# Kernel optimization log

Measured on AMD Instinct MI355X. Metric: run time of the kernel, lower is better.

The kernel has to match this reference:

```python
import jax, jax.numpy as jnp
import numpy as np

D = 256                      # covariance dim, hardcoded by bottleneck Conv2d(_, 256, 1)
ITER_N = 5                   # SqrtmLayer(output, 5)
_r, _c = np.triu_indices(D)
FLAT_IDX = jnp.asarray(_r * D + _c)   # upper-tri (incl. diag) indices into flattened d*d


def setup_inputs() -> dict:
    key = jax.random.key(0)
    ks = jax.random.split(key, 5)
    B, C, H, W = 64, 2048, 16, 16
    num_classes = 4
    feats = D * (D + 1) // 2  # 32896
    return {
        "features": jax.random.normal(ks[0], (B, C, H, W), jnp.float32),
        "w_bn": jax.random.normal(ks[1], (D, C), jnp.float32) * 0.02,
        "b_bn": jnp.zeros((D,), jnp.float32),
        "w_type": jax.random.normal(ks[2], (num_classes, feats), jnp.float32) * 0.01,
        "b_type": jnp.zeros((num_classes,), jnp.float32),
        "w_flag": jax.random.normal(ks[3], (1, feats), jnp.float32) * 0.01,
        "b_flag": jnp.zeros((1,), jnp.float32),
    }


def _covpool(x):
    # x: [B, d, h, w] -> second-order pooling: x_f @ I_hat @ x_f^T, equivalent
    # to (1/M) * centered @ centered^T  (I_hat = -1/M^2 * ones + 1/M * eye)
    B, d, h, w = x.shape
    M = h * w
    xf = x.reshape(B, d, M)
    centered = xf - xf.mean(axis=2, keepdims=True)
    return jnp.einsum('bim,bjm->bij', centered, centered) / M  # [B, d, d]


def _sqrtm_ns(A, iter_n=ITER_N):
    # Newton-Schulz iteration for matrix square root (iSQRT-COV style)
    B, d, _ = A.shape
    I3 = 3.0 * jnp.eye(d, dtype=A.dtype)
    normA = jnp.trace(A, axis1=1, axis2=2)          # [B], pre-normalization
    An = A / normA[:, None, None]
    ZY = 0.5 * (I3 - An)
    Y = jnp.matmul(An, ZY)
    Z = ZY
    for _ in range(iter_n - 2):
        ZY = 0.5 * (I3 - jnp.matmul(Z, Y))
        Y = jnp.matmul(Y, ZY)
        Z = jnp.matmul(ZY, Z)
    YZY = 0.5 * jnp.matmul(Y, I3 - jnp.matmul(Z, Y))
    return YZY * jnp.sqrt(normA)[:, None, None]     # post-compensation


def reference(features, w_bn, b_bn, w_type, b_type, w_flag, b_flag):
    # 1x1 bottleneck conv: [B, C, H, W] -> [B, 256, H, W]
    x = jnp.einsum('bchw,oc->bohw', features, w_bn) + b_bn[None, :, None, None]
    cov = _covpool(x)                # [B, 256, 256]
    s = _sqrtm_ns(cov)               # [B, 256, 256]
    B = s.shape[0]
    vec = s.reshape(B, D * D)[:, FLAT_IDX]   # triu-vec: [B, 32896]
    type_logits = vec @ w_type.T + b_type    # [B, num_classes]
    flag_logits = vec @ w_flag.T + b_flag    # [B, 1]
    return (type_logits, flag_logits)
```

## Files before the change

### kernel.cpp

```cpp
#include <hip/hip_runtime.h>
#include <math.h>


typedef __attribute__((ext_vector_type(8))) short bf16x8;
typedef __attribute__((ext_vector_type(4))) float f32x4;
typedef __attribute__((ext_vector_type(4))) unsigned u32x4;
typedef __attribute__((ext_vector_type(2))) unsigned u32x2;

__device__ __forceinline__ unsigned fbits(float f) { union { float f; unsigned u; } x; x.f = f; return x.u; }
__device__ __forceinline__ float bitsf(unsigned u) { union { float f; unsigned u; } x; x.u = u; return x.f; }
__device__ __forceinline__ float bf16v(short h) { return bitsf(((unsigned)(unsigned short)h) << 16); }

__device__ __forceinline__ unsigned pack_h(float a, float b) {
  return (fbits(a) >> 16) | (fbits(b) & 0xFFFF0000u);
}
__device__ __forceinline__ unsigned pack_l(float a, float b) {
  float la = a - bitsf(fbits(a) & 0xFFFF0000u);
  float lb = b - bitsf(fbits(b) & 0xFFFF0000u);
  return (fbits(la) >> 16) | (fbits(lb) & 0xFFFF0000u);
}

__device__ __forceinline__ const bf16x8* fragp(const char* M, int kt, int row,
                                               int g, int pl) {
  return (const bf16x8*)(M + (size_t)kt * 32768 + (size_t)row * 128 +
                         ((((pl << 2) + g) ^ (row & 7)) << 4));
}
__device__ __forceinline__ const bf16x8* fragl(const char* L, int kt, int row,
                                               int g, int pl) {
  return (const bf16x8*)(L + kt * 8192 + row * 128 +
                         ((((pl << 2) + g) ^ (row & 7)) << 4));
}

__device__ __forceinline__ void write_quad_g(char* M, int row, int k0,
                                             const float* v) {
  char* rp = M + (size_t)(k0 >> 5) * 32768 + (size_t)row * 128;
  const int s = (k0 & 31) >> 3, bo = (k0 & 7) * 2;
  *(u32x2*)(rp + (((s) ^ (row & 7)) << 4) + bo) =
      (u32x2){pack_h(v[0], v[1]), pack_h(v[2], v[3])};
  *(u32x2*)(rp + (((s + 4) ^ (row & 7)) << 4) + bo) =
      (u32x2){pack_l(v[0], v[1]), pack_l(v[2], v[3])};
}
__device__ __forceinline__ void write_quad_l(char* L, int row, int k0,
                                             const float* v) {
  char* rp = L + (k0 >> 5) * 8192 + row * 128;
  const int s = (k0 & 31) >> 3, bo = (k0 & 7) * 2;
  *(u32x2*)(rp + (((s) ^ (row & 7)) << 4) + bo) =
      (u32x2){pack_h(v[0], v[1]), pack_h(v[2], v[3])};
  *(u32x2*)(rp + (((s + 4) ^ (row & 7)) << 4) + bo) =
      (u32x2){pack_l(v[0], v[1]), pack_l(v[2], v[3])};
}
__device__ __forceinline__ void read_quad_g(const char* M, int row, int k0,
                                            float* v) {
  const char* rp = M + (size_t)(k0 >> 5) * 32768 + (size_t)row * 128;
  const int s = (k0 & 31) >> 3, bo = (k0 & 7) * 2;
  const u32x2 hq = *(const u32x2*)(rp + (((s) ^ (row & 7)) << 4) + bo);
  const u32x2 lq = *(const u32x2*)(rp + (((s + 4) ^ (row & 7)) << 4) + bo);
  v[0] = bitsf(hq[0] << 16) + bitsf(lq[0] << 16);
  v[1] = bitsf(hq[0] & 0xFFFF0000u) + bitsf(lq[0] & 0xFFFF0000u);
  v[2] = bitsf(hq[1] << 16) + bitsf(lq[1] << 16);
  v[3] = bitsf(hq[1] & 0xFFFF0000u) + bitsf(lq[1] & 0xFFFF0000u);
}

#define MFMA3(c, aH, aL, bH, bL)                                            \
  c = __builtin_amdgcn_mfma_f32_16x16x32_bf16(aL, bH, c, 0, 0, 0);          \
  c = __builtin_amdgcn_mfma_f32_16x16x32_bf16(aH, bL, c, 0, 0, 0);          \
  c = __builtin_amdgcn_mfma_f32_16x16x32_bf16(aH, bH, c, 0, 0, 0);

#define LGKM_BAR() do { asm volatile("s_waitcnt lgkmcnt(0)" ::: "memory"); \
                        __builtin_amdgcn_s_barrier(); } while (0)

__global__ __launch_bounds__(256) void prep_k(
    const float* __restrict__ w_bn, const float* __restrict__ w_type,
    const float* __restrict__ w_flag, char* __restrict__ Wf,
    float* __restrict__ W2)
{
  const int bid = blockIdx.x;
  if (bid < 64) {
    const int kt = bid, r = threadIdx.x;
    const float* src = w_bn + (size_t)r * 2048 + kt * 32;
    char* rp = Wf + (size_t)kt * 32768 + (size_t)r * 128;
#pragma unroll
    for (int s = 0; s < 4; ++s) {
      float x[8];
#pragma unroll
      for (int e = 0; e < 8; ++e) x[e] = src[s * 8 + e];
      *(u32x4*)(rp + ((s ^ (r & 7)) << 4)) =
          (u32x4){pack_h(x[0], x[1]), pack_h(x[2], x[3]),
                  pack_h(x[4], x[5]), pack_h(x[6], x[7])};
      *(u32x4*)(rp + (((s + 4) ^ (r & 7)) << 4)) =
          (u32x4){pack_l(x[0], x[1]), pack_l(x[2], x[3]),
                  pack_l(x[4], x[5]), pack_l(x[6], x[7])};
    }
  } else {
    const int idx = bid - 64;
    const int v = idx >> 6, chunk = idx & 63;
    const float* src = (v < 4) ? (w_type + (size_t)v * 32896) : w_flag;
    const int e0 = chunk * 1024 + threadIdx.x * 4;
#pragma unroll
    for (int q = 0; q < 4; ++q) {
      const int e = e0 + q;
      const int i = e >> 8, j = e & 255;
      const int r = i < j ? i : j, c = i < j ? j : i;
      const int t = r * 256 - (r * (r - 1)) / 2 + (c - r);
      W2[(size_t)v * 65536 + e] = src[t] * (i == j ? 1.0f : 0.5f);
    }
  }
}

__global__ __launch_bounds__(512) void conv6_k(
    const char* __restrict__ Wf, const float* __restrict__ F,
    float* __restrict__ Xpart)
{
  __shared__ float bf32s[2][64 * 33];
  __shared__ __align__(16) char bfmt[2][2][8192];

  const int tid = threadIdx.x, lane = tid & 63, w = tid >> 6;
  const int wr = w >> 1, wc = w & 1, fr = lane & 15, g = lane >> 4;
  const int jb = blockIdx.x * 64, bz = blockIdx.y, ks = blockIdx.z;
  const int kb = ks * 32;
  const float* Fb = F + (size_t)bz * 524288;

  const int blc = tid >> 4, blpx = (tid & 15) * 4;
  const int pkpx = tid >> 3, pkq = tid & 3, pkpl = (tid >> 2) & 1;

  f32x4 acc[4][2] = {};
  bf16x8 paA[4][2], paB[4][2];

  auto bload = [&](int t) -> float4 {
    return *(const float4*)(Fb + ((size_t)(kb + t) * 32 + blc) * 256 + jb + blpx);
  };
  auto bf32w = [&](int kk, const float4& r) {
    float* p = &bf32s[kk][0];
    p[(blpx + 0) * 33 + blc] = r.x;
    p[(blpx + 1) * 33 + blc] = r.y;
    p[(blpx + 2) * 33 + blc] = r.z;
    p[(blpx + 3) * 33 + blc] = r.w;
  };
  auto aload = [&](int t, bf16x8 (*pa)[2]) {
#pragma unroll
    for (int m = 0; m < 4; ++m) {
      const int r = wr * 64 + m * 16 + fr;
#pragma unroll
      for (int pl = 0; pl < 2; ++pl) pa[m][pl] = *fragp(Wf, kb + t, r, g, pl);
    }
  };
  auto pack = [&](int kk, int dq) {
    const float* p = &bf32s[kk][pkpx * 33 + pkq * 8];
    float x[8];
#pragma unroll
    for (int e = 0; e < 8; ++e) x[e] = p[e];
    u32x4 outv;
    if (pkpl == 0)
      outv = (u32x4){pack_h(x[0], x[1]), pack_h(x[2], x[3]),
                     pack_h(x[4], x[5]), pack_h(x[6], x[7])};
    else
      outv = (u32x4){pack_l(x[0], x[1]), pack_l(x[2], x[3]),
                     pack_l(x[4], x[5]), pack_l(x[6], x[7])};
    const int slot = ((pkpl << 2) + pkq) ^ (pkpx & 7);
    *(u32x4*)(&bfmt[dq][kk][pkpx * 128 + slot * 16]) = outv;
  };
  auto gemmstep = [&](int sq, int kk, bf16x8 (*pa)[2]) {
    bf16x8 bH[2], bL[2];
#pragma unroll
    for (int n = 0; n < 2; ++n) {
      const int r = wc * 32 + n * 16 + fr;
      const char* rp = &bfmt[sq][kk][r * 128];
      bH[n] = *(const bf16x8*)(rp + ((g ^ (r & 7)) << 4));
      bL[n] = *(const bf16x8*)(rp + (((g + 4) ^ (r & 7)) << 4));
    }
#pragma unroll
    for (int m = 0; m < 4; ++m)
#pragma unroll
      for (int n = 0; n < 2; ++n) {
        f32x4 c = acc[m][n];
        MFMA3(c, pa[m][0], pa[m][1], bH[n], bL[n]);
        acc[m][n] = c;
      }
  };

  float4 b0 = bload(0), b1 = bload(1), b2 = bload(2), b3 = bload(3);
  float4 blE0 = bload(4), blE1 = bload(5);
  float4 blO0 = bload(6), blO1 = bload(7);
  aload(0, paA);
  aload(1, paB);

  bf32w(0, b0); bf32w(1, b1);
  LGKM_BAR();
  pack(0, 0); pack(1, 0);
  LGKM_BAR();
  bf32w(0, b2); bf32w(1, b3);
  LGKM_BAR();

  for (int pp = 0; pp < 8; ++pp) {
    const int k4 = 4 * pp;
    gemmstep(0, 0, paA);
    gemmstep(0, 1, paB);
    aload(k4 + 2, paA);
    aload(k4 + 3, paB);
    pack(0, 1); pack(1, 1);
    LGKM_BAR();
    if (pp < 7) { bf32w(0, blE0); bf32w(1, blE1); }
    if (pp < 6) { blE0 = bload(k4 + 8); blE1 = bload(k4 + 9); }
    LGKM_BAR();
    gemmstep(1, 0, paA);
    gemmstep(1, 1, paB);
    if (pp < 7) { aload(k4 + 4, paA); aload(k4 + 5, paB); }
    if (pp < 7) { pack(0, 0); pack(1, 0); }
    LGKM_BAR();
    if (pp < 7) { bf32w(0, blO0); bf32w(1, blO1); }
    if (pp < 6) { blO0 = bload(k4 + 10); blO1 = bload(k4 + 11); }
    LGKM_BAR();
  }

  float* Xp = Xpart + ((size_t)ks * 64 + bz) * 65536;
#pragma unroll
  for (int m = 0; m < 4; ++m) {
    const int gi0 = wr * 64 + m * 16 + g * 4;
#pragma unroll
    for (int n = 0; n < 2; ++n) {
      const int gj = jb + wc * 32 + n * 16 + fr;
#pragma unroll
      for (int j = 0; j < 4; ++j)
        Xp[(size_t)(gi0 + j) * 256 + gj] = acc[m][n][j];
    }
  }
}

__global__ __launch_bounds__(256) void combine_k(
    const float* __restrict__ Xp0, const float* __restrict__ Xp1,
    const float* __restrict__ bias, char* __restrict__ X,
    float* __restrict__ mu, float* __restrict__ nrm_part)
{
  const int chunk = blockIdx.x, bz = blockIdx.y;
  const int tid = threadIdx.x, lane = tid & 63, w = tid >> 6;
  const float* p0 = Xp0 + (size_t)bz * 65536;
  const float* p1 = Xp1 + (size_t)bz * 65536;
  char* Xb = X + (size_t)bz * 262144;
  float tracc = 0.f;
#pragma unroll
  for (int i = 0; i < 8; ++i) {
    const int r = chunk * 32 + w * 8 + i;
    const float4 a = *(const float4*)(p0 + (size_t)r * 256 + lane * 4);
    const float4 b = *(const float4*)(p1 + (size_t)r * 256 + lane * 4);
    const float bi = bias[r];
    float v[4] = {a.x + b.x + bi, a.y + b.y + bi,
                  a.z + b.z + bi, a.w + b.w + bi};
    float s = v[0] + v[1] + v[2] + v[3];
    float ss = v[0] * v[0] + v[1] * v[1] + v[2] * v[2] + v[3] * v[3];
#pragma unroll
    for (int o = 32; o > 0; o >>= 1) {
      s += __shfl_down(s, o);
      ss += __shfl_down(ss, o);
    }
    const float st = __shfl(s, 0), sst = __shfl(ss, 0);
    const float m = st * (1.f / 256.f);
    if (lane == 0) mu[bz * 256 + r] = m;
    tracc += sst * (1.f / 256.f) - m * m;
    write_quad_g(Xb, r, lane * 4, v);
  }
  __shared__ float red[4];
  if (lane == 0) red[w] = tracc;
  __syncthreads();
  if (tid == 0)
    nrm_part[bz * 8 + chunk] = red[0] + red[1] + red[2] + red[3];
}

__device__ __forceinline__ float nrm_sum(const float* nrmp, int bz) {
  float nv = 0.f;
#pragma unroll
  for (int q = 0; q < 8; ++q) nv += nrmp[bz * 8 + q];
  return nv;
}

template <int MODE>
__global__ __launch_bounds__(512) void col_k(
    const char* __restrict__ A1, const char* __restrict__ Bsrc,
    const char* __restrict__ Ys, const char* __restrict__ Zs,
    char* __restrict__ outA, char* __restrict__ outB,
    const float* __restrict__ mu, const float* __restrict__ nrmp,
    float* __restrict__ Sf)
{
  __shared__ __align__(16) char Plds[65536];
  const int tid = threadIdx.x, lane = tid & 63, w = tid >> 6;
  const int fr = lane & 15, g = lane >> 4;
  const int blk = blockIdx.x;
  const int bz = (blk & 7) * 8 + ((blk >> 3) & 7);
  const int jb = (blk >> 6) * 64;
  const size_t MB = 262144;
  const char* Ab = A1 + (size_t)bz * MB;
  const char* Bb = Bsrc + (size_t)bz * MB;
  const int r0 = g * 4;

  f32x4 acc[2][4] = {};
  {
    bf16x8 pa[2][2][2], pb[2][4][2];
#pragma unroll
    for (int par = 0; par < 2; ++par) {
#pragma unroll
      for (int m = 0; m < 2; ++m) {
        const int r = w * 32 + m * 16 + fr;
#pragma unroll
        for (int pl = 0; pl < 2; ++pl) pa[par][m][pl] = *fragp(Ab, par, r, g, pl);
      }
#pragma unroll
      for (int n = 0; n < 4; ++n) {
        const int r = jb + n * 16 + fr;
#pragma unroll
        for (int pl = 0; pl < 2; ++pl) pb[par][n][pl] = *fragp(Bb, par, r, g, pl);
      }
    }
    for (int t2 = 0; t2 < 8; t2 += 2) {
#pragma unroll
      for (int par = 0; par < 2; ++par) {
        const int t = t2 + par;
        bf16x8 aH[2], aL[2], bH[4], bL[4];
#pragma unroll
        for (int m = 0; m < 2; ++m) { aH[m] = pa[par][m][0]; aL[m] = pa[par][m][1]; }
#pragma unroll
        for (int n = 0; n < 4; ++n) { bH[n] = pb[par][n][0]; bL[n] = pb[par][n][1]; }
        if (t + 2 < 8) {
#pragma unroll
          for (int m = 0; m < 2; ++m) {
            const int r = w * 32 + m * 16 + fr;
#pragma unroll
            for (int pl = 0; pl < 2; ++pl)
              pa[par][m][pl] = *fragp(Ab, t + 2, r, g, pl);
          }
#pragma unroll
          for (int n = 0; n < 4; ++n) {
            const int r = jb + n * 16 + fr;
#pragma unroll
            for (int pl = 0; pl < 2; ++pl)
              pb[par][n][pl] = *fragp(Bb, t + 2, r, g, pl);
          }
        }
#pragma unroll
        for (int m = 0; m < 2; ++m)
#pragma unroll
          for (int n = 0; n < 4; ++n) {
            f32x4 c = acc[m][n];
            MFMA3(c, aH[m], aL[m], bH[n], bL[n]);
            acc[m][n] = c;
          }
      }
    }
  }

  if constexpr (MODE == 0) {
    const float rn = 1.0f / nrm_sum(nrmp, bz);
    const float* mub = mu + bz * 256;
    char* oA = outA + (size_t)bz * MB;
    char* oB = outB + (size_t)bz * MB;
#pragma unroll
    for (int m = 0; m < 2; ++m) {
      const int gi0 = w * 32 + m * 16 + r0;
#pragma unroll
      for (int n = 0; n < 4; ++n) {
        const int gj = jb + n * 16 + fr;
        float vv[4], zz[4];
#pragma unroll
        for (int j = 0; j < 4; ++j) {
          const float v =
              (acc[m][n][j] * (1.f / 256.f) - mub[gi0 + j] * mub[gj]) * rn;
          vv[j] = v;
          zz[j] = (gi0 + j == gj ? 1.5f : 0.f) - 0.5f * v;
        }
        write_quad_g(oA, gj, gi0, vv);
        write_quad_g(oB, gj, gi0, zz);
      }
    }
  } else if constexpr (MODE == 1) {
    char* oA = outA + (size_t)bz * MB;
#pragma unroll
    for (int m = 0; m < 2; ++m) {
      const int gi0 = w * 32 + m * 16 + r0;
#pragma unroll
      for (int n = 0; n < 4; ++n) {
        const int gj = jb + n * 16 + fr;
        float av[4], vv[4];
        read_quad_g(Bb, gj, gi0, av);
#pragma unroll
        for (int j = 0; j < 4; ++j) vv[j] = 1.5f * av[j] - 0.5f * acc[m][n][j];
        write_quad_g(oA, gj, gi0, vv);
      }
    }
  } else {
#pragma unroll
    for (int m = 0; m < 2; ++m) {
      const int gi0 = w * 32 + m * 16 + r0;
#pragma unroll
      for (int n = 0; n < 4; ++n) {
        const int jl = n * 16 + fr;
        float vv[4] = {acc[m][n][0], acc[m][n][1], acc[m][n][2], acc[m][n][3]};
        write_quad_l(Plds, jl, gi0, vv);
      }
    }
    const char* Yb = Ys + (size_t)bz * MB;
    const char* Zb = (MODE == 2) ? (Zs + (size_t)bz * MB) : nullptr;
    bf16x8 py[2][2][2], pz[2][2][2];
#pragma unroll
    for (int par = 0; par < 2; ++par)
#pragma unroll
      for (int m = 0; m < 2; ++m) {
        const int r = w * 32 + m * 16 + fr;
#pragma unroll
        for (int pl = 0; pl < 2; ++pl) {
          py[par][m][pl] = *fragp(Yb, par, r, g, pl);
          if constexpr (MODE == 2) pz[par][m][pl] = *fragp(Zb, par, r, g, pl);
        }
      }
    __syncthreads();

    f32x4 aY[2][4] = {}, aZ[2][4] = {};
    for (int t2 = 0; t2 < 8; t2 += 2) {
#pragma unroll
      for (int par = 0; par < 2; ++par) {
        const int t = t2 + par;
        bf16x8 yH[2], yL[2], zH[2], zL[2];
#pragma unroll
        for (int m = 0; m < 2; ++m) {
          yH[m] = py[par][m][0]; yL[m] = py[par][m][1];
          if constexpr (MODE == 2) { zH[m] = pz[par][m][0]; zL[m] = pz[par][m][1]; }
        }
        if (t + 2 < 8) {
#pragma unroll
          for (int m = 0; m < 2; ++m) {
            const int r = w * 32 + m * 16 + fr;
#pragma unroll
            for (int pl = 0; pl < 2; ++pl) {
              py[par][m][pl] = *fragp(Yb, t + 2, r, g, pl);
              if constexpr (MODE == 2) pz[par][m][pl] = *fragp(Zb, t + 2, r, g, pl);
            }
          }
        }
        bf16x8 bH[4], bL[4];
#pragma unroll
        for (int n = 0; n < 4; ++n) {
          const int jl = n * 16 + fr;
          bH[n] = *fragl(Plds, t, jl, g, 0);
          bL[n] = *fragl(Plds, t, jl, g, 1);
        }
#pragma unroll
        for (int m = 0; m < 2; ++m)
#pragma unroll
          for (int n = 0; n < 4; ++n) {
            f32x4 cy = aY[m][n];
            MFMA3(cy, yH[m], yL[m], bH[n], bL[n]);
            aY[m][n] = cy;
            if constexpr (MODE == 2) {
              f32x4 cz = aZ[m][n];
              MFMA3(cz, zH[m], zL[m], bH[n], bL[n]);
              aZ[m][n] = cz;
            }
          }
      }
    }
    if constexpr (MODE == 2) {
      char* oA = outA + (size_t)bz * MB;
      char* oB = outB + (size_t)bz * MB;
#pragma unroll
      for (int m = 0; m < 2; ++m) {
        const int gi0 = w * 32 + m * 16 + r0;
#pragma unroll
        for (int n = 0; n < 4; ++n) {
          const int gj = jb + n * 16 + fr;
          float base[4], vv[4];
          read_quad_g(Yb, gj, gi0, base);
#pragma unroll
          for (int j = 0; j < 4; ++j) vv[j] = 1.5f * base[j] - 0.5f * aY[m][n][j];
          write_quad_g(oA, gj, gi0, vv);
          read_quad_g(Zb, gj, gi0, base);
#pragma unroll
          for (int j = 0; j < 4; ++j) vv[j] = 1.5f * base[j] - 0.5f * aZ[m][n][j];
          write_quad_g(oB, gj, gi0, vv);
        }
      }
    } else {
      const float sq = sqrtf(nrm_sum(nrmp, bz));
      float* Sb = Sf + (size_t)bz * 65536;
#pragma unroll
      for (int m = 0; m < 2; ++m) {
        const int gi0 = w * 32 + m * 16 + r0;
#pragma unroll
        for (int n = 0; n < 4; ++n) {
          const int gj = jb + n * 16 + fr;
          float base[4];
          read_quad_g(Yb, gj, gi0, base);
          f32x4 vv;
#pragma unroll
          for (int j = 0; j < 4; ++j)
            vv[j] = (1.5f * base[j] - 0.5f * aY[m][n][j]) * sq;
          *(f32x4*)(Sb + (size_t)gj * 256 + gi0) = vv;
        }
      }
    }
  }
}

__global__ __launch_bounds__(256) void head2(
    const float* __restrict__ Sf, const float* __restrict__ W2,
    const float* __restrict__ b_type, const float* __restrict__ b_flag,
    float* __restrict__ out)
{
  const int b = blockIdx.x, v = blockIdx.y, tid = threadIdx.x;
  const float4* s4 = (const float4*)(Sf + (size_t)b * 65536);
  const float4* w4 = (const float4*)(W2 + (size_t)v * 65536);
  float acc = 0.f;
  for (int i = tid; i < 16384; i += 256) {
    const float4 a = s4[i], c = w4[i];
    acc += a.x * c.x + a.y * c.y + a.z * c.z + a.w * c.w;
  }
  __shared__ float red[256];
  red[tid] = acc;
  __syncthreads();
  for (int o = 128; o > 0; o >>= 1) {
    if (tid < o) red[tid] += red[tid + o];
    __syncthreads();
  }
  if (tid == 0) {
    if (v < 4) out[b * 4 + v] = red[0] + b_type[v];
    else       out[256 + b] = red[0] + b_flag[0];
  }
}

extern "C" void kernel_launch(void* const* d_in, const int* in_sizes, int n_in,
                              void* d_out, int out_size, void* d_ws, size_t ws_size,
                              hipStream_t stream)
{
  const float* features = (const float*)d_in[0];
  const float* w_bn     = (const float*)d_in[1];
  const float* b_bn     = (const float*)d_in[2];
  const float* w_type   = (const float*)d_in[3];
  const float* b_type   = (const float*)d_in[4];
  const float* w_flag   = (const float*)d_in[5];
  const float* b_flag   = (const float*)d_in[6];
  float* out = (float*)d_out;

  char* W = (char*)d_ws;
  const size_t PB = 16777216;
  char* P0 = W;           char* P1 = W + PB;     char* P2 = W + 2 * PB;
  char* P3 = W + 3 * PB;  char* P4 = W + 4 * PB;
  char* Wf = W + 5 * PB;
  float* W2 = (float*)(W + 5 * PB + 2097152);
  float* mu = (float*)(W + 5 * PB + 4194304);
  float* nrm_part = mu + 16384;
  float* Xpart = (float*)(W + 5 * PB + 8388608);
  float* Sf = (float*)P4;

  prep_k<<<dim3(384), dim3(256), 0, stream>>>(w_bn, w_type, w_flag, Wf, W2);
  conv6_k<<<dim3(4, 64, 2), dim3(512), 0, stream>>>(Wf, features, Xpart);
  combine_k<<<dim3(8, 64), dim3(256), 0, stream>>>(
      Xpart, Xpart + 64ull * 65536, b_bn, P0, mu, nrm_part);

  const dim3 cg(256), cb(512);
  col_k<0><<<cg, cb, 0, stream>>>(P0, P0, nullptr, nullptr, P1, P2, mu, nrm_part, nullptr);
  col_k<1><<<cg, cb, 0, stream>>>(P1, P1, nullptr, nullptr, P3, nullptr, nullptr, nullptr, nullptr);
  col_k<2><<<cg, cb, 0, stream>>>(P2, P3, P3, P2, P0, P4, nullptr, nullptr, nullptr);
  col_k<2><<<cg, cb, 0, stream>>>(P4, P0, P0, P4, P1, P2, nullptr, nullptr, nullptr);
  col_k<2><<<cg, cb, 0, stream>>>(P2, P1, P1, P2, P3, P0, nullptr, nullptr, nullptr);
  col_k<3><<<cg, cb, 0, stream>>>(P0, P3, P3, nullptr, nullptr, nullptr, nullptr, nrm_part, Sf);

  head2<<<dim3(64, 5), dim3(256), 0, stream>>>(Sf, W2, b_type, b_flag, out);
  (void)in_sizes; (void)n_in; (void)out_size; (void)ws_size;
}
```

Baseline: 274.4 us.

## Halve col_k column tile to double grid, permute W2 to match coalesced S writes

Each col_k block now covers 32 output columns instead of 64, so the grid grows from 256 to 512 blocks and LDS use per block halves, which spreads the Newton-Schulz matmuls over more CUs. The final-stage S output is written in a per-thread contiguous layout instead of row-major. prep_k permutes the head weights W2 into that same order so head2's dot product stays correct. The cost is that A-side fragments are reloaded by twice as many blocks, and the prep indexing becomes more complex.

```diff
diff --git a/kernel.cpp b/kernel.cpp
--- a/kernel.cpp
+++ b/kernel.cpp
@@ -25,9 +25,9 @@
   return (const bf16x8*)(M + (size_t)kt * 32768 + (size_t)row * 128 +
                          ((((pl << 2) + g) ^ (row & 7)) << 4));
 }
-__device__ __forceinline__ const bf16x8* fragl(const char* L, int kt, int row,
-                                               int g, int pl) {
-  return (const bf16x8*)(L + kt * 8192 + row * 128 +
+__device__ __forceinline__ const bf16x8* fragl32(const char* L, int kt, int row,
+                                                 int g, int pl) {
+  return (const bf16x8*)(L + kt * 4096 + row * 128 +
                          ((((pl << 2) + g) ^ (row & 7)) << 4));
 }
 
@@ -40,9 +40,9 @@
   *(u32x2*)(rp + (((s + 4) ^ (row & 7)) << 4) + bo) =
       (u32x2){pack_l(v[0], v[1]), pack_l(v[2], v[3])};
 }
-__device__ __forceinline__ void write_quad_l(char* L, int row, int k0,
-                                             const float* v) {
-  char* rp = L + (k0 >> 5) * 8192 + row * 128;
+__device__ __forceinline__ void write_quad_l32(char* L, int row, int k0,
+                                               const float* v) {
+  char* rp = L + (k0 >> 5) * 4096 + row * 128;
   const int s = (k0 & 31) >> 3, bo = (k0 & 7) * 2;
   *(u32x2*)(rp + (((s) ^ (row & 7)) << 4) + bo) =
       (u32x2){pack_h(v[0], v[1]), pack_h(v[2], v[3])};
@@ -93,17 +93,27 @@
     }
   } else {
     const int idx = bid - 64;
-    const int v = idx >> 6, chunk = idx & 63;
+    const int v = idx >> 4, chunk = idx & 15;
     const float* src = (v < 4) ? (w_type + (size_t)v * 32896) : w_flag;
-    const int e0 = chunk * 1024 + threadIdx.x * 4;
-#pragma unroll
-    for (int q = 0; q < 4; ++q) {
-      const int e = e0 + q;
-      const int i = e >> 8, j = e & 255;
-      const int r = i < j ? i : j, c = i < j ? j : i;
-      const int t = r * 256 - (r * (r - 1)) / 2 + (c - r);
-      W2[(size_t)v * 65536 + e] = src[t] * (i == j ? 1.0f : 0.5f);
-    }
+    const int s0 = chunk * 4096 + threadIdx.x * 16;
+    float outv[16];
+#pragma unroll
+    for (int q = 0; q < 16; ++q) {
+      const int s = s0 + q;
+      const int jbp = s >> 13, r = s & 8191;
+      const int ttid = r >> 4, qq = r & 15;
+      const int m = qq >> 3, n = (qq >> 2) & 1, jj = qq & 3;
+      const int ww = ttid >> 6, ll = ttid & 63;
+      const int i = ww * 32 + m * 16 + (ll >> 4) * 4 + jj;
+      const int jcol = jbp * 32 + n * 16 + (ll & 15);
+      const int rr = i < jcol ? i : jcol, cc = i < jcol ? jcol : i;
+      const int t = rr * 256 - (rr * (rr - 1)) / 2 + (cc - rr);
+      outv[q] = src[t] * (i == jcol ? 1.0f : 0.5f);
+    }
+    float* dst = W2 + (size_t)v * 65536 + s0;
+#pragma unroll
+    for (int q = 0; q < 4; ++q)
+      *(f32x4*)(dst + q * 4) = *(f32x4*)(outv + q * 4);
   }
 }
 
@@ -280,20 +290,21 @@
     const float* __restrict__ mu, const float* __restrict__ nrmp,
     float* __restrict__ Sf)
 {
-  __shared__ __align__(16) char Plds[65536];
+  __shared__ __align__(16) char Plds[32768];
   const int tid = threadIdx.x, lane = tid & 63, w = tid >> 6;
   const int fr = lane & 15, g = lane >> 4;
   const int blk = blockIdx.x;
   const int bz = (blk & 7) * 8 + ((blk >> 3) & 7);
-  const int jb = (blk >> 6) * 64;
+  const int jbp = blk >> 6;
+  const int jb = jbp * 32;
   const size_t MB = 262144;
   const char* Ab = A1 + (size_t)bz * MB;
   const char* Bb = Bsrc + (size_t)bz * MB;
   const int r0 = g * 4;
 
-  f32x4 acc[2][4] = {};
+  f32x4 acc[2][2] = {};
   {
-    bf16x8 pa[2][2][2], pb[2][4][2];
+    bf16x8 pa[2][2][2], pb[2][2][2];
 #pragma unroll
     for (int par = 0; par < 2; ++par) {
 #pragma unroll
@@ -303,7 +314,7 @@
         for (int pl = 0; pl < 2; ++pl) pa[par][m][pl] = *fragp(Ab, par, r, g, pl);
       }
 #pragma unroll
-      for (int n = 0; n < 4; ++n) {
+      for (int n = 0; n < 2; ++n) {
         const int r = jb + n * 16 + fr;
 #pragma unroll
         for (int pl = 0; pl < 2; ++pl) pb[par][n][pl] = *fragp(Bb, par, r, g, pl);
@@ -313,11 +324,11 @@
 #pragma unroll
       for (int par = 0; par < 2; ++par) {
         const int t = t2 + par;
-        bf16x8 aH[2], aL[2], bH[4], bL[4];
+        bf16x8 aH[2], aL[2], bH[2], bL[2];
 #pragma unroll
         for (int m = 0; m < 2; ++m) { aH[m] = pa[par][m][0]; aL[m] = pa[par][m][1]; }
 #pragma unroll
-        for (int n = 0; n < 4; ++n) { bH[n] = pb[par][n][0]; bL[n] = pb[par][n][1]; }
+        for (int n = 0; n < 2; ++n) { bH[n] = pb[par][n][0]; bL[n] = pb[par][n][1]; }
         if (t + 2 < 8) {
 #pragma unroll
           for (int m = 0; m < 2; ++m) {
@@ -327,7 +338,7 @@
               pa[par][m][pl] = *fragp(Ab, t + 2, r, g, pl);
           }
 #pragma unroll
-          for (int n = 0; n < 4; ++n) {
+          for (int n = 0; n < 2; ++n) {
             const int r = jb + n * 16 + fr;
 #pragma unroll
             for (int pl = 0; pl < 2; ++pl)
@@ -337,7 +348,7 @@
 #pragma unroll
         for (int m = 0; m < 2; ++m)
 #pragma unroll
-          for (int n = 0; n < 4; ++n) {
+          for (int n = 0; n < 2; ++n) {
             f32x4 c = acc[m][n];
             MFMA3(c, aH[m], aL[m], bH[n], bL[n]);
             acc[m][n] = c;
@@ -355,7 +366,7 @@
     for (int m = 0; m < 2; ++m) {
       const int gi0 = w * 32 + m * 16 + r0;
 #pragma unroll
-      for (int n = 0; n < 4; ++n) {
+      for (int n = 0; n < 2; ++n) {
         const int gj = jb + n * 16 + fr;
         float vv[4], zz[4];
 #pragma unroll
@@ -375,7 +386,7 @@
     for (int m = 0; m < 2; ++m) {
       const int gi0 = w * 32 + m * 16 + r0;
 #pragma unroll
-      for (int n = 0; n < 4; ++n) {
+      for (int n = 0; n < 2; ++n) {
         const int gj = jb + n * 16 + fr;
         float av[4], vv[4];
         read_quad_g(Bb, gj, gi0, av);
@@ -389,10 +400,10 @@
     for (int m = 0; m < 2; ++m) {
       const int gi0 = w * 32 + m * 16 + r0;
 #pragma unroll
-      for (int n = 0; n < 4; ++n) {
+      for (int n = 0; n < 2; ++n) {
         const int jl = n * 16 + fr;
         float vv[4] = {acc[m][n][0], acc[m][n][1], acc[m][n][2], acc[m][n][3]};
-        write_quad_l(Plds, jl, gi0, vv);
+        write_quad_l32(Plds, jl, gi0, vv);
       }
     }
     const char* Yb = Ys + (size_t)bz * MB;
@@ -411,7 +422,7 @@
       }
     __syncthreads();
 
-    f32x4 aY[2][4] = {}, aZ[2][4] = {};
+    f32x4 aY[2][2] = {}, aZ[2][2] = {};
     for (int t2 = 0; t2 < 8; t2 += 2) {
 #pragma unroll
       for (int par = 0; par < 2; ++par) {
@@ -433,17 +444,17 @@
             }
           }
         }
-        bf16x8 bH[4], bL[4];
-#pragma unroll
-        for (int n = 0; n < 4; ++n) {
+        bf16x8 bH[2], bL[2];
+#pragma unroll
+        for (int n = 0; n < 2; ++n) {
           const int jl = n * 16 + fr;
-          bH[n] = *fragl(Plds, t, jl, g, 0);
-          bL[n] = *fragl(Plds, t, jl, g, 1);
+          bH[n] = *fragl32(Plds, t, jl, g, 0);
+          bL[n] = *fragl32(Plds, t, jl, g, 1);
         }
 #pragma unroll
         for (int m = 0; m < 2; ++m)
 #pragma unroll
-          for (int n = 0; n < 4; ++n) {
+          for (int n = 0; n < 2; ++n) {
             f32x4 cy = aY[m][n];
             MFMA3(cy, yH[m], yL[m], bH[n], bL[n]);
             aY[m][n] = cy;
@@ -462,7 +473,7 @@
       for (int m = 0; m < 2; ++m) {
         const int gi0 = w * 32 + m * 16 + r0;
 #pragma unroll
-        for (int n = 0; n < 4; ++n) {
+        for (int n = 0; n < 2; ++n) {
           const int gj = jb + n * 16 + fr;
           float base[4], vv[4];
           read_quad_g(Yb, gj, gi0, base);
@@ -477,12 +488,12 @@
       }
     } else {
       const float sq = sqrtf(nrm_sum(nrmp, bz));
-      float* Sb = Sf + (size_t)bz * 65536;
+      float* Sb = Sf + (size_t)bz * 65536 + (size_t)jbp * 8192 + (size_t)tid * 16;
 #pragma unroll
       for (int m = 0; m < 2; ++m) {
         const int gi0 = w * 32 + m * 16 + r0;
 #pragma unroll
-        for (int n = 0; n < 4; ++n) {
+        for (int n = 0; n < 2; ++n) {
           const int gj = jb + n * 16 + fr;
           float base[4];
           read_quad_g(Yb, gj, gi0, base);
@@ -490,7 +501,7 @@
 #pragma unroll
           for (int j = 0; j < 4; ++j)
             vv[j] = (1.5f * base[j] - 0.5f * aY[m][n][j]) * sq;
-          *(f32x4*)(Sb + (size_t)gj * 256 + gi0) = vv;
+          *(f32x4*)(Sb + m * 8 + n * 4) = vv;
         }
       }
     }
@@ -547,12 +558,12 @@
   float* Xpart = (float*)(W + 5 * PB + 8388608);
   float* Sf = (float*)P4;
 
-  prep_k<<<dim3(384), dim3(256), 0, stream>>>(w_bn, w_type, w_flag, Wf, W2);
+  prep_k<<<dim3(144), dim3(256), 0, stream>>>(w_bn, w_type, w_flag, Wf, W2);
   conv6_k<<<dim3(4, 64, 2), dim3(512), 0, stream>>>(Wf, features, Xpart);
   combine_k<<<dim3(8, 64), dim3(256), 0, stream>>>(
       Xpart, Xpart + 64ull * 65536, b_bn, P0, mu, nrm_part);
 
-  const dim3 cg(256), cb(512);
+  const dim3 cg(512), cb(512);
   col_k<0><<<cg, cb, 0, stream>>>(P0, P0, nullptr, nullptr, P1, P2, mu, nrm_part, nullptr);
   col_k<1><<<cg, cb, 0, stream>>>(P1, P1, nullptr, nullptr, P3, nullptr, nullptr, nullptr, nullptr);
   col_k<2><<<cg, cb, 0, stream>>>(P2, P3, P3, P2, P0, P4, nullptr, nullptr, nullptr);
```

After: 286.2 us. 1.04x slower.

## Split col_k row range across two blocks and permute head weights to match output layout

Applied to the files above, without the earlier changes.

Doubles the col_k grid from 256 to 512 blocks by splitting each 64-column tile's 256 output rows into two 128-row halves, so each wave computes 16 rows instead of 32. This raises parallelism and occupancy on the GPU's many CUs, at the cost of reloading the B operand twice and, in modes 2/3, recomputing the stage-1 product for the full tile in each half. The final Sf store is rewritten as contiguous per-thread writes in a fragment-ordered layout, and prep_k permutes W2 into the same order so head2's dot product stays correct. The stage-1 redundancy in modes 2 and 3 adds MFMA work.

```diff
diff --git a/kernel.cpp b/kernel.cpp
--- a/kernel.cpp
+++ b/kernel.cpp
@@ -9,7 +9,6 @@
 
 __device__ __forceinline__ unsigned fbits(float f) { union { float f; unsigned u; } x; x.f = f; return x.u; }
 __device__ __forceinline__ float bitsf(unsigned u) { union { float f; unsigned u; } x; x.u = u; return x.f; }
-__device__ __forceinline__ float bf16v(short h) { return bitsf(((unsigned)(unsigned short)h) << 16); }
 
 __device__ __forceinline__ unsigned pack_h(float a, float b) {
   return (fbits(a) >> 16) | (fbits(b) & 0xFFFF0000u);
@@ -93,17 +92,26 @@
     }
   } else {
     const int idx = bid - 64;
-    const int v = idx >> 6, chunk = idx & 63;
+    const int v = idx >> 4, chunk = idx & 15;
     const float* src = (v < 4) ? (w_type + (size_t)v * 32896) : w_flag;
-    const int e0 = chunk * 1024 + threadIdx.x * 4;
-#pragma unroll
-    for (int q = 0; q < 4; ++q) {
-      const int e = e0 + q;
-      const int i = e >> 8, j = e & 255;
-      const int r = i < j ? i : j, c = i < j ? j : i;
-      const int t = r * 256 - (r * (r - 1)) / 2 + (c - r);
-      W2[(size_t)v * 65536 + e] = src[t] * (i == j ? 1.0f : 0.5f);
-    }
+    const int s0 = chunk * 4096 + threadIdx.x * 16;
+    float outv[16];
+#pragma unroll
+    for (int q = 0; q < 16; ++q) {
+      const int s = s0 + q;
+      const int jbp = s >> 14, rh = (s >> 13) & 1;
+      const int ttid = (s >> 4) & 511, n = (s >> 2) & 3, jj = s & 3;
+      const int ww = ttid >> 6, ll = ttid & 63;
+      const int i = rh * 128 + ww * 16 + ((ll >> 4) << 2) + jj;
+      const int jcol = jbp * 64 + n * 16 + (ll & 15);
+      const int rr = i < jcol ? i : jcol, cc = i < jcol ? jcol : i;
+      const int t = rr * 256 - (rr * (rr - 1)) / 2 + (cc - rr);
+      outv[q] = src[t] * (i == jcol ? 1.0f : 0.5f);
+    }
+    float* dst = W2 + (size_t)v * 65536 + s0;
+#pragma unroll
+    for (int q = 0; q < 4; ++q)
+      *(f32x4*)(dst + q * 4) = *(f32x4*)(outv + q * 4);
   }
 }
 
@@ -285,23 +293,33 @@
   const int fr = lane & 15, g = lane >> 4;
   const int blk = blockIdx.x;
   const int bz = (blk & 7) * 8 + ((blk >> 3) & 7);
-  const int jb = (blk >> 6) * 64;
+  const int jbp = (blk >> 6) & 3;
+  const int rh = blk >> 8;
+  const int jb = jbp * 64;
   const size_t MB = 262144;
   const char* Ab = A1 + (size_t)bz * MB;
   const char* Bb = Bsrc + (size_t)bz * MB;
   const int r0 = g * 4;
 
-  f32x4 acc[2][4] = {};
+  constexpr int S1M = (MODE <= 1) ? 1 : 2;
+  auto s1row = [&](int m) {
+    if constexpr (MODE <= 1) return rh * 128 + w * 16 + fr;
+    else return w * 32 + m * 16 + fr;
+  };
+
+  f32x4 acc[S1M][4];
+#pragma unroll
+  for (int m = 0; m < S1M; ++m)
+#pragma unroll
+    for (int n = 0; n < 4; ++n) acc[m][n] = (f32x4){0.f, 0.f, 0.f, 0.f};
   {
-    bf16x8 pa[2][2][2], pb[2][4][2];
+    bf16x8 pa[2][S1M][2], pb[2][4][2];
 #pragma unroll
     for (int par = 0; par < 2; ++par) {
 #pragma unroll
-      for (int m = 0; m < 2; ++m) {
-        const int r = w * 32 + m * 16 + fr;
-#pragma unroll
-        for (int pl = 0; pl < 2; ++pl) pa[par][m][pl] = *fragp(Ab, par, r, g, pl);
-      }
+      for (int m = 0; m < S1M; ++m)
+#pragma unroll
+        for (int pl = 0; pl < 2; ++pl) pa[par][m][pl] = *fragp(Ab, par, s1row(m), g, pl);
 #pragma unroll
       for (int n = 0; n < 4; ++n) {
         const int r = jb + n * 16 + fr;
@@ -313,19 +331,17 @@
 #pragma unroll
       for (int par = 0; par < 2; ++par) {
         const int t = t2 + par;
-        bf16x8 aH[2], aL[2], bH[4], bL[4];
-#pragma unroll
-        for (int m = 0; m < 2; ++m) { aH[m] = pa[par][m][0]; aL[m] = pa[par][m][1]; }
+        bf16x8 aH[S1M], aL[S1M], bH[4], bL[4];
+#pragma unroll
+        for (int m = 0; m < S1M; ++m) { aH[m] = pa[par][m][0]; aL[m] = pa[par][m][1]; }
 #pragma unroll
         for (int n = 0; n < 4; ++n) { bH[n] = pb[par][n][0]; bL[n] = pb[par][n][1]; }
         if (t + 2 < 8) {
 #pragma unroll
-          for (int m = 0; m < 2; ++m) {
-            const int r = w * 32 + m * 16 + fr;
+          for (int m = 0; m < S1M; ++m)
 #pragma unroll
             for (int pl = 0; pl < 2; ++pl)
-              pa[par][m][pl] = *fragp(Ab, t + 2, r, g, pl);
-          }
+              pa[par][m][pl] = *fragp(Ab, t + 2, s1row(m), g, pl);
 #pragma unroll
           for (int n = 0; n < 4; ++n) {
             const int r = jb + n * 16 + fr;
@@ -335,7 +351,7 @@
           }
         }
 #pragma unroll
-        for (int m = 0; m < 2; ++m)
+        for (int m = 0; m < S1M; ++m)
 #pragma unroll
           for (int n = 0; n < 4; ++n) {
             f32x4 c = acc[m][n];
@@ -351,38 +367,32 @@
     const float* mub = mu + bz * 256;
     char* oA = outA + (size_t)bz * MB;
     char* oB = outB + (size_t)bz * MB;
-#pragma unroll
-    for (int m = 0; m < 2; ++m) {
-      const int gi0 = w * 32 + m * 16 + r0;
-#pragma unroll
-      for (int n = 0; n < 4; ++n) {
-        const int gj = jb + n * 16 + fr;
-        float vv[4], zz[4];
-#pragma unroll
-        for (int j = 0; j < 4; ++j) {
-          const float v =
-              (acc[m][n][j] * (1.f / 256.f) - mub[gi0 + j] * mub[gj]) * rn;
-          vv[j] = v;
-          zz[j] = (gi0 + j == gj ? 1.5f : 0.f) - 0.5f * v;
-        }
-        write_quad_g(oA, gj, gi0, vv);
-        write_quad_g(oB, gj, gi0, zz);
-      }
+    const int gi0 = rh * 128 + w * 16 + r0;
+#pragma unroll
+    for (int n = 0; n < 4; ++n) {
+      const int gj = jb + n * 16 + fr;
+      float vv[4], zz[4];
+#pragma unroll
+      for (int j = 0; j < 4; ++j) {
+        const float v =
+            (acc[0][n][j] * (1.f / 256.f) - mub[gi0 + j] * mub[gj]) * rn;
+        vv[j] = v;
+        zz[j] = (gi0 + j == gj ? 1.5f : 0.f) - 0.5f * v;
+      }
+      write_quad_g(oA, gj, gi0, vv);
+      write_quad_g(oB, gj, gi0, zz);
     }
   } else if constexpr (MODE == 1) {
     char* oA = outA + (size_t)bz * MB;
-#pragma unroll
-    for (int m = 0; m < 2; ++m) {
-      const int gi0 = w * 32 + m * 16 + r0;
-#pragma unroll
-      for (int n = 0; n < 4; ++n) {
-        const int gj = jb + n * 16 + fr;
-        float av[4], vv[4];
-        read_quad_g(Bb, gj, gi0, av);
-#pragma unroll
-        for (int j = 0; j < 4; ++j) vv[j] = 1.5f * av[j] - 0.5f * acc[m][n][j];
-        write_quad_g(oA, gj, gi0, vv);
-      }
+    const int gi0 = rh * 128 + w * 16 + r0;
+#pragma unroll
+    for (int n = 0; n < 4; ++n) {
+      const int gj = jb + n * 16 + fr;
+      float av[4], vv[4];
+      read_quad_g(Bb, gj, gi0, av);
+#pragma unroll
+      for (int j = 0; j < 4; ++j) vv[j] = 1.5f * av[j] - 0.5f * acc[0][n][j];
+      write_quad_g(oA, gj, gi0, vv);
     }
   } else {
 #pragma unroll
@@ -397,40 +407,29 @@
     }
     const char* Yb = Ys + (size_t)bz * MB;
     const char* Zb = (MODE == 2) ? (Zs + (size_t)bz * MB) : nullptr;
-    bf16x8 py[2][2][2], pz[2][2][2];
+    const int s2r = rh * 128 + w * 16 + fr;
+    bf16x8 py[2][2], pz[2][2];
 #pragma unroll
     for (int par = 0; par < 2; ++par)
 #pragma unroll
-      for (int m = 0; m < 2; ++m) {
-        const int r = w * 32 + m * 16 + fr;
-#pragma unroll
-        for (int pl = 0; pl < 2; ++pl) {
-          py[par][m][pl] = *fragp(Yb, par, r, g, pl);
-          if constexpr (MODE == 2) pz[par][m][pl] = *fragp(Zb, par, r, g, pl);
-        }
+      for (int pl = 0; pl < 2; ++pl) {
+        py[par][pl] = *fragp(Yb, par, s2r, g, pl);
+        if constexpr (MODE == 2) pz[par][pl] = *fragp(Zb, par, s2r, g, pl);
       }
     __syncthreads();
 
-    f32x4 aY[2][4] = {}, aZ[2][4] = {};
+    f32x4 aY[4] = {}, aZ[4] = {};
     for (int t2 = 0; t2 < 8; t2 += 2) {
 #pragma unroll
       for (int par = 0; par < 2; ++par) {
         const int t = t2 + par;
-        bf16x8 yH[2], yL[2], zH[2], zL[2];
-#pragma unroll
-        for (int m = 0; m < 2; ++m) {
-          yH[m] = py[par][m][0]; yL[m] = py[par][m][1];
-          if constexpr (MODE == 2) { zH[m] = pz[par][m][0]; zL[m] = pz[par][m][1]; }
-        }
+        bf16x8 yH = py[par][0], yL = py[par][1], zH, zL;
+        if constexpr (MODE == 2) { zH = pz[par][0]; zL = pz[par][1]; }
         if (t + 2 < 8) {
 #pragma unroll
-          for (int m = 0; m < 2; ++m) {
-            const int r = w * 32 + m * 16 + fr;
-#pragma unroll
-            for (int pl = 0; pl < 2; ++pl) {
-              py[par][m][pl] = *fragp(Yb, t + 2, r, g, pl);
-              if constexpr (MODE == 2) pz[par][m][pl] = *fragp(Zb, t + 2, r, g, pl);
-            }
+          for (int pl = 0; pl < 2; ++pl) {
+            py[par][pl] = *fragp(Yb, t + 2, s2r, g, pl);
+            if constexpr (MODE == 2) pz[par][pl] = *fragp(Zb, t + 2, s2r, g, pl);
           }
         }
         bf16x8 bH[4], bL[4];
@@ -441,57 +440,49 @@
           bL[n] = *fragl(Plds, t, jl, g, 1);
         }
 #pragma unroll
-        for (int m = 0; m < 2; ++m)
-#pragma unroll
-          for (int n = 0; n < 4; ++n) {
-            f32x4 cy = aY[m][n];
-            MFMA3(cy, yH[m], yL[m], bH[n], bL[n]);
-            aY[m][n] = cy;
-            if constexpr (MODE == 2) {
-              f32x4 cz = aZ[m][n];
-              MFMA3(cz, zH[m], zL[m], bH[n], bL[n]);
-              aZ[m][n] = cz;
-            }
+        for (int n = 0; n < 4; ++n) {
+          f32x4 cy = aY[n];
+          MFMA3(cy, yH, yL, bH[n], bL[n]);
+          aY[n] = cy;
+          if constexpr (MODE == 2) {
+            f32x4 cz = aZ[n];
+            MFMA3(cz, zH, zL, bH[n], bL[n]);
+            aZ[n] = cz;
           }
-      }
-    }
+        }
+      }
+    }
+    const int gi0 = rh * 128 + w * 16 + r0;
     if constexpr (MODE == 2) {
       char* oA = outA + (size_t)bz * MB;
       char* oB = outB + (size_t)bz * MB;
 #pragma unroll
-      for (int m = 0; m < 2; ++m) {
-        const int gi0 = w * 32 + m * 16 + r0;
-#pragma unroll
-        for (int n = 0; n < 4; ++n) {
-          const int gj = jb + n * 16 + fr;
-          float base[4], vv[4];
-          read_quad_g(Yb, gj, gi0, base);
-#pragma unroll
-          for (int j = 0; j < 4; ++j) vv[j] = 1.5f * base[j] - 0.5f * aY[m][n][j];
-          write_quad_g(oA, gj, gi0, vv);
-          read_quad_g(Zb, gj, gi0, base);
-#pragma unroll
-          for (int j = 0; j < 4; ++j) vv[j] = 1.5f * base[j] - 0.5f * aZ[m][n][j];
-          write_quad_g(oB, gj, gi0, vv);
-        }
+      for (int n = 0; n < 4; ++n) {
+        const int gj = jb + n * 16 + fr;
+        float base[4], vv[4];
+        read_quad_g(Yb, gj, gi0, base);
+#pragma unroll
+        for (int j = 0; j < 4; ++j) vv[j] = 1.5f * base[j] - 0.5f * aY[n][j];
+        write_quad_g(oA, gj, gi0, vv);
+        read_quad_g(Zb, gj, gi0, base);
+#pragma unroll
+        for (int j = 0; j < 4; ++j) vv[j] = 1.5f * base[j] - 0.5f * aZ[n][j];
+        write_quad_g(oB, gj, gi0, vv);
       }
     } else {
       const float sq = sqrtf(nrm_sum(nrmp, bz));
-      float* Sb = Sf + (size_t)bz * 65536;
-#pragma unroll
-      for (int m = 0; m < 2; ++m) {
-        const int gi0 = w * 32 + m * 16 + r0;
-#pragma unroll
-        for (int n = 0; n < 4; ++n) {
-          const int gj = jb + n * 16 + fr;
-          float base[4];
-          read_quad_g(Yb, gj, gi0, base);
-          f32x4 vv;
-#pragma unroll
-          for (int j = 0; j < 4; ++j)
-            vv[j] = (1.5f * base[j] - 0.5f * aY[m][n][j]) * sq;
-          *(f32x4*)(Sb + (size_t)gj * 256 + gi0) = vv;
-        }
+      float* Sb = Sf + (size_t)bz * 65536 + (size_t)jbp * 16384 +
+                  (size_t)rh * 8192 + (size_t)tid * 16;
+#pragma unroll
+      for (int n = 0; n < 4; ++n) {
+        const int gj = jb + n * 16 + fr;
+        float base[4];
+        read_quad_g(Yb, gj, gi0, base);
+        f32x4 vv;
+#pragma unroll
+        for (int j = 0; j < 4; ++j)
+          vv[j] = (1.5f * base[j] - 0.5f * aY[n][j]) * sq;
+        *(f32x4*)(Sb + n * 4) = vv;
       }
     }
   }
@@ -547,12 +538,12 @@
   float* Xpart = (float*)(W + 5 * PB + 8388608);
   float* Sf = (float*)P4;
 
-  prep_k<<<dim3(384), dim3(256), 0, stream>>>(w_bn, w_type, w_flag, Wf, W2);
+  prep_k<<<dim3(144), dim3(256), 0, stream>>>(w_bn, w_type, w_flag, Wf, W2);
   conv6_k<<<dim3(4, 64, 2), dim3(512), 0, stream>>>(Wf, features, Xpart);
   combine_k<<<dim3(8, 64), dim3(256), 0, stream>>>(
       Xpart, Xpart + 64ull * 65536, b_bn, P0, mu, nrm_part);
 
-  const dim3 cg(256), cb(512);
+  const dim3 cg(512), cb(512);
   col_k<0><<<cg, cb, 0, stream>>>(P0, P0, nullptr, nullptr, P1, P2, mu, nrm_part, nullptr);
   col_k<1><<<cg, cb, 0, stream>>>(P1, P1, nullptr, nullptr, P3, nullptr, nullptr, nullptr, nullptr);
   col_k<2><<<cg, cb, 0, stream>>>(P2, P3, P3, P2, P0, P4, nullptr, nullptr, nullptr);
```

After: 293.6 us. 1.07x slower.

## Drop An output, compute Y from ZY algebraically, write S in fragment order

Applied to the files above, without the earlier changes.

The first kernel stops writing the normalized matrix An and emits only ZY. The next kernel computes Y = An·ZY as 3·ZY − 2·ZY² using An = 3I − 2ZY, which cuts one full-matrix write per batch. The final sqrtm kernel writes S contiguously in MFMA fragment order, and prep_k permutes the head weights W2 into the same order, so the stores are coalesced and the dot product in the head stays correct. The buffer rotation is remapped to match, and rewriting ZY² in place of An·ZY slightly changes the rounding.

```diff
diff --git a/kernel.cpp b/kernel.cpp
--- a/kernel.cpp
+++ b/kernel.cpp
@@ -9,7 +9,6 @@
 
 __device__ __forceinline__ unsigned fbits(float f) { union { float f; unsigned u; } x; x.f = f; return x.u; }
 __device__ __forceinline__ float bitsf(unsigned u) { union { float f; unsigned u; } x; x.u = u; return x.f; }
-__device__ __forceinline__ float bf16v(short h) { return bitsf(((unsigned)(unsigned short)h) << 16); }
 
 __device__ __forceinline__ unsigned pack_h(float a, float b) {
   return (fbits(a) >> 16) | (fbits(b) & 0xFFFF0000u);
@@ -93,17 +92,27 @@
     }
   } else {
     const int idx = bid - 64;
-    const int v = idx >> 6, chunk = idx & 63;
+    const int v = idx >> 4, chunk = idx & 15;
     const float* src = (v < 4) ? (w_type + (size_t)v * 32896) : w_flag;
-    const int e0 = chunk * 1024 + threadIdx.x * 4;
-#pragma unroll
-    for (int q = 0; q < 4; ++q) {
-      const int e = e0 + q;
-      const int i = e >> 8, j = e & 255;
-      const int r = i < j ? i : j, c = i < j ? j : i;
-      const int t = r * 256 - (r * (r - 1)) / 2 + (c - r);
-      W2[(size_t)v * 65536 + e] = src[t] * (i == j ? 1.0f : 0.5f);
-    }
+    const int s0 = chunk * 4096 + threadIdx.x * 16;
+    float outv[16];
+#pragma unroll
+    for (int q = 0; q < 16; ++q) {
+      const int s = s0 + q;
+      const int jbp = s >> 14, r = s & 16383;
+      const int ttid = r >> 5, qq = r & 31;
+      const int m = qq >> 4, n = (qq >> 2) & 3, jj = qq & 3;
+      const int ww = ttid >> 6, ll = ttid & 63;
+      const int i = ww * 32 + m * 16 + (ll >> 4) * 4 + jj;
+      const int jcol = jbp * 64 + n * 16 + (ll & 15);
+      const int rr = i < jcol ? i : jcol, cc = i < jcol ? jcol : i;
+      const int t = rr * 256 - (rr * (rr - 1)) / 2 + (cc - rr);
+      outv[q] = src[t] * (i == jcol ? 1.0f : 0.5f);
+    }
+    float* dst = W2 + (size_t)v * 65536 + s0;
+#pragma unroll
+    for (int q = 0; q < 4; ++q)
+      *(f32x4*)(dst + q * 4) = *(f32x4*)(outv + q * 4);
   }
 }
 
@@ -285,7 +294,8 @@
   const int fr = lane & 15, g = lane >> 4;
   const int blk = blockIdx.x;
   const int bz = (blk & 7) * 8 + ((blk >> 3) & 7);
-  const int jb = (blk >> 6) * 64;
+  const int jbp = blk >> 6;
+  const int jb = jbp * 64;
   const size_t MB = 262144;
   const char* Ab = A1 + (size_t)bz * MB;
   const char* Bb = Bsrc + (size_t)bz * MB;
@@ -349,7 +359,6 @@
   if constexpr (MODE == 0) {
     const float rn = 1.0f / nrm_sum(nrmp, bz);
     const float* mub = mu + bz * 256;
-    char* oA = outA + (size_t)bz * MB;
     char* oB = outB + (size_t)bz * MB;
 #pragma unroll
     for (int m = 0; m < 2; ++m) {
@@ -357,15 +366,13 @@
 #pragma unroll
       for (int n = 0; n < 4; ++n) {
         const int gj = jb + n * 16 + fr;
-        float vv[4], zz[4];
+        float zz[4];
 #pragma unroll
         for (int j = 0; j < 4; ++j) {
           const float v =
               (acc[m][n][j] * (1.f / 256.f) - mub[gi0 + j] * mub[gj]) * rn;
-          vv[j] = v;
           zz[j] = (gi0 + j == gj ? 1.5f : 0.f) - 0.5f * v;
         }
-        write_quad_g(oA, gj, gi0, vv);
         write_quad_g(oB, gj, gi0, zz);
       }
     }
@@ -377,10 +384,10 @@
 #pragma unroll
       for (int n = 0; n < 4; ++n) {
         const int gj = jb + n * 16 + fr;
-        float av[4], vv[4];
-        read_quad_g(Bb, gj, gi0, av);
-#pragma unroll
-        for (int j = 0; j < 4; ++j) vv[j] = 1.5f * av[j] - 0.5f * acc[m][n][j];
+        float zv[4], vv[4];
+        read_quad_g(Bb, gj, gi0, zv);
+#pragma unroll
+        for (int j = 0; j < 4; ++j) vv[j] = 3.f * zv[j] - 2.f * acc[m][n][j];
         write_quad_g(oA, gj, gi0, vv);
       }
     }
@@ -477,7 +484,7 @@
       }
     } else {
       const float sq = sqrtf(nrm_sum(nrmp, bz));
-      float* Sb = Sf + (size_t)bz * 65536;
+      float* Sb = Sf + (size_t)bz * 65536 + (size_t)jbp * 16384 + (size_t)tid * 32;
 #pragma unroll
       for (int m = 0; m < 2; ++m) {
         const int gi0 = w * 32 + m * 16 + r0;
@@ -490,7 +497,7 @@
 #pragma unroll
           for (int j = 0; j < 4; ++j)
             vv[j] = (1.5f * base[j] - 0.5f * aY[m][n][j]) * sq;
-          *(f32x4*)(Sb + (size_t)gj * 256 + gi0) = vv;
+          *(f32x4*)(Sb + m * 16 + n * 4) = vv;
         }
       }
     }
@@ -547,18 +554,18 @@
   float* Xpart = (float*)(W + 5 * PB + 8388608);
   float* Sf = (float*)P4;
 
-  prep_k<<<dim3(384), dim3(256), 0, stream>>>(w_bn, w_type, w_flag, Wf, W2);
+  prep_k<<<dim3(144), dim3(256), 0, stream>>>(w_bn, w_type, w_flag, Wf, W2);
   conv6_k<<<dim3(4, 64, 2), dim3(512), 0, stream>>>(Wf, features, Xpart);
   combine_k<<<dim3(8, 64), dim3(256), 0, stream>>>(
       Xpart, Xpart + 64ull * 65536, b_bn, P0, mu, nrm_part);
 
   const dim3 cg(256), cb(512);
-  col_k<0><<<cg, cb, 0, stream>>>(P0, P0, nullptr, nullptr, P1, P2, mu, nrm_part, nullptr);
-  col_k<1><<<cg, cb, 0, stream>>>(P1, P1, nullptr, nullptr, P3, nullptr, nullptr, nullptr, nullptr);
-  col_k<2><<<cg, cb, 0, stream>>>(P2, P3, P3, P2, P0, P4, nullptr, nullptr, nullptr);
-  col_k<2><<<cg, cb, 0, stream>>>(P4, P0, P0, P4, P1, P2, nullptr, nullptr, nullptr);
-  col_k<2><<<cg, cb, 0, stream>>>(P2, P1, P1, P2, P3, P0, nullptr, nullptr, nullptr);
-  col_k<3><<<cg, cb, 0, stream>>>(P0, P3, P3, nullptr, nullptr, nullptr, nullptr, nrm_part, Sf);
+  col_k<0><<<cg, cb, 0, stream>>>(P0, P0, nullptr, nullptr, nullptr, P2, mu, nrm_part, nullptr);
+  col_k<1><<<cg, cb, 0, stream>>>(P2, P2, nullptr, nullptr, P3, nullptr, nullptr, nullptr, nullptr);
+  col_k<2><<<cg, cb, 0, stream>>>(P2, P3, P3, P2, P0, P1, nullptr, nullptr, nullptr);
+  col_k<2><<<cg, cb, 0, stream>>>(P1, P0, P0, P1, P3, P2, nullptr, nullptr, nullptr);
+  col_k<2><<<cg, cb, 0, stream>>>(P2, P3, P3, P2, P1, P0, nullptr, nullptr, nullptr);
+  col_k<3><<<cg, cb, 0, stream>>>(P0, P1, P1, nullptr, nullptr, nullptr, nullptr, nrm_part, Sf);
 
   head2<<<dim3(64, 5), dim3(256), 0, stream>>>(Sf, W2, b_type, b_flag, out);
   (void)in_sizes; (void)n_in; (void)out_size; (void)ws_size;
```

Result: faster. 268.7 us, median of 2 (-2.0%).
